# Kernel optimization log

Hardware: AMD Instinct MI355X
Metric: run time of the kernel (lower is better)

Reference implementation:

```python
import jax, jax.numpy as jnp
import numpy as np

PROP_TIME = 8  # matches init kwarg prop_time


def setup_inputs() -> dict:
    key = jax.random.key(0)
    k1, k2, k3, k4, k5 = jax.random.split(key, 5)
    B, H, W = 8, 480, 640
    return {
        "guided1": jax.random.normal(k1, (B, 9, H, W), dtype=jnp.float32),
        "guided2": jax.random.normal(k2, (B, 9, H, W), dtype=jnp.float32),
        "guided3": jax.random.normal(k3, (B, 9, H, W), dtype=jnp.float32),
        "fuse": jax.random.uniform(k4, (B, 3, H, W), dtype=jnp.float32),
        "x": jax.random.normal(k5, (B, 1, H, W), dtype=jnp.float32),
    }


def _neighbors(x, d):
    """Gather the 3x3 dilated neighborhood of a [B,1,H,W] map -> [B,9,H,W].
    Equivalent to F.unfold(x, 3, dilation=d, padding=d) reshaped to spatial."""
    B, _, H, W = x.shape
    xp = jnp.pad(x[:, 0], ((0, 0), (d, d), (d, d)))  # B, H+2d, W+2d
    return jnp.stack(
        [xp[:, i * d:i * d + H, j * d:j * d + W] for i in range(3) for j in range(3)],
        axis=1,
    )


def reference(guided1, guided2, guided3, fuse, x):
    # per-pixel affinity kernels, normalized over the 9 taps
    k1 = jax.nn.softmax(guided1, axis=1)
    k2 = jax.nn.softmax(guided2, axis=1)
    k3 = jax.nn.softmax(guided3, axis=1)
    f1, f2, f3 = fuse[:, 0:1], fuse[:, 1:2], fuse[:, 2:3]
    for _ in range(PROP_TIME):
        o1 = jnp.sum(_neighbors(x, 1) * k1, axis=1, keepdims=True)  # B,1,H,W
        o2 = jnp.sum(_neighbors(x, 2) * k2, axis=1, keepdims=True)
        o3 = jnp.sum(_neighbors(x, 3) * k3, axis=1, keepdims=True)
        x = o1 * f1 + o2 * f2 + o3 * f3
    return x
```

## Files before the change

### kernel.cpp

```cpp
#include <hip/hip_runtime.h>

constexpr int B_ = 8;
constexpr int H_ = 480;
constexpr int W_ = 640;
constexpr int HW = H_ * W_;
constexpr int N  = B_ * HW;

__global__ __launch_bounds__(256) void wprep_kernel(
    const float* __restrict__ g1, const float* __restrict__ g2,
    const float* __restrict__ g3, const float* __restrict__ fuse,
    _Float16* __restrict__ w)
{
    const int j  = blockIdx.x * 64 + (threadIdx.x & 63);
    const int i  = blockIdx.y * 4  + (threadIdx.x >> 6);
    const int z  = blockIdx.z;
    const int b  = z / 3;
    const int d  = z - b * 3;
    const int hw = i * W_ + j;
    const int p  = b * HW + hw;

    const float* gs[3] = {g1, g2, g3};
    const float* gb = gs[d] + (size_t)b * 9 * HW + hw;

    float e[9];
    float m = -1e30f;
#pragma unroll
    for (int c = 0; c < 9; ++c) {
        e[c] = gb[(size_t)c * HW];
        m = fmaxf(m, e[c]);
    }
    float s = 0.f;
#pragma unroll
    for (int c = 0; c < 9; ++c) {
        e[c] = __expf(e[c] - m);
        s += e[c];
    }
    const float f = fuse[((size_t)b * 3 + d) * HW + hw] / s;
#pragma unroll
    for (int c = 0; c < 9; ++c)
        w[(size_t)(d * 9 + c) * N + p] = (_Float16)(e[c] * f);
}

__global__ __launch_bounds__(256) void prop_kernel(
    const float* __restrict__ xin, const _Float16* __restrict__ w,
    float* __restrict__ xout)
{
    const int j  = blockIdx.x * 64 + (threadIdx.x & 63);
    const int i  = blockIdx.y * 4  + (threadIdx.x >> 6);
    const int b  = blockIdx.z;
    const int hw = i * W_ + j;
    const int p  = b * HW + hw;

    const float* xb = xin + (size_t)b * HW;
    float acc = 0.f;
#pragma unroll
    for (int d = 1; d <= 3; ++d) {
#pragma unroll
        for (int ki = 0; ki < 3; ++ki) {
            const int ii = i + (ki - 1) * d;
            const bool vi = (unsigned)ii < (unsigned)H_;
#pragma unroll
            for (int kj = 0; kj < 3; ++kj) {
                const int jj = j + (kj - 1) * d;
                float xv = 0.f;
                if (vi && (unsigned)jj < (unsigned)W_)
                    xv = xb[ii * W_ + jj];
                const int plane = (d - 1) * 9 + ki * 3 + kj;
                acc = fmaf(xv, (float)w[(size_t)plane * N + p], acc);
            }
        }
    }
    xout[p] = acc;
}

extern "C" void kernel_launch(void* const* d_in, const int* in_sizes, int n_in,
                              void* d_out, int out_size, void* d_ws, size_t ws_size,
                              hipStream_t stream)
{
    const float* g1   = (const float*)d_in[0];
    const float* g2   = (const float*)d_in[1];
    const float* g3   = (const float*)d_in[2];
    const float* fuse = (const float*)d_in[3];
    const float* x    = (const float*)d_in[4];
    float* out = (float*)d_out;

    char* ws = (char*)d_ws;
    _Float16* w = (_Float16*)ws;
    float* xa = (float*)(ws + (size_t)27 * N * 2);
    float* xb = xa + N;

    const dim3 block(256);
    wprep_kernel<<<dim3(W_ / 64, H_ / 4, B_ * 3), block, 0, stream>>>(g1, g2, g3, fuse, w);

    const dim3 pgrid(W_ / 64, H_ / 4, B_);
    const float* src = x;
    float* bufs[2] = {xa, xb};
    for (int t = 0; t < 8; ++t) {
        float* dst = (t == 7) ? out : bufs[t & 1];
        prop_kernel<<<pgrid, block, 0, stream>>>(src, w, dst);
        src = dst;
    }
}
```

Measured before the change: 297.7 us.

## Store per-pixel weights interleaved (28 halves) and load them with vector loads

Changes the weight workspace from 27 planar fp16 planes to a pixel-interleaved layout padded to 28 halves, so each pixel's weights sit contiguously. The prep kernel now computes all three softmaxes per pixel and writes them with 16-byte vector stores. The propagation kernel loads the weights with three 16-byte loads and one 8-byte load instead of 27 scattered 2-byte loads. This cuts the number of memory transactions, but each lane's weight loads are now strided by 56 bytes across the wave, which may reduce coalescing efficiency.

Result: no change. 301.8 us (+1.4%).

```diff
diff --git a/kernel.cpp b/kernel.cpp
--- a/kernel.cpp
+++ b/kernel.cpp
@@ -1,44 +1,56 @@
 #include <hip/hip_runtime.h>
+
+typedef __attribute__((ext_vector_type(4))) float    float4v;
+typedef __attribute__((ext_vector_type(8))) _Float16 half8v;
+typedef __attribute__((ext_vector_type(4))) _Float16 half4v;
 
 constexpr int B_ = 8;
 constexpr int H_ = 480;
 constexpr int W_ = 640;
 constexpr int HW = H_ * W_;
 constexpr int N  = B_ * HW;
+constexpr int WPP = 28;
 
 __global__ __launch_bounds__(256) void wprep_kernel(
     const float* __restrict__ g1, const float* __restrict__ g2,
     const float* __restrict__ g3, const float* __restrict__ fuse,
     _Float16* __restrict__ w)
 {
-    const int j  = blockIdx.x * 64 + (threadIdx.x & 63);
-    const int i  = blockIdx.y * 4  + (threadIdx.x >> 6);
-    const int z  = blockIdx.z;
-    const int b  = z / 3;
-    const int d  = z - b * 3;
-    const int hw = i * W_ + j;
-    const int p  = b * HW + hw;
+    const int p  = blockIdx.x * 256 + threadIdx.x;
+    const int b  = p / HW;
+    const int hw = p - b * HW;
+
+    _Float16 wl[WPP];
+    wl[27] = (_Float16)0.f;
 
     const float* gs[3] = {g1, g2, g3};
-    const float* gb = gs[d] + (size_t)b * 9 * HW + hw;
+#pragma unroll
+    for (int d = 0; d < 3; ++d) {
+        const float* gb = gs[d] + (size_t)b * 9 * HW + hw;
+        float e[9];
+        float m = -1e30f;
+#pragma unroll
+        for (int c = 0; c < 9; ++c) {
+            e[c] = gb[(size_t)c * HW];
+            m = fmaxf(m, e[c]);
+        }
+        float s = 0.f;
+#pragma unroll
+        for (int c = 0; c < 9; ++c) {
+            e[c] = __expf(e[c] - m);
+            s += e[c];
+        }
+        const float f = fuse[((size_t)b * 3 + d) * HW + hw] / s;
+#pragma unroll
+        for (int c = 0; c < 9; ++c)
+            wl[d * 9 + c] = (_Float16)(e[c] * f);
+    }
 
-    float e[9];
-    float m = -1e30f;
-#pragma unroll
-    for (int c = 0; c < 9; ++c) {
-        e[c] = gb[(size_t)c * HW];
-        m = fmaxf(m, e[c]);
-    }
-    float s = 0.f;
-#pragma unroll
-    for (int c = 0; c < 9; ++c) {
-        e[c] = __expf(e[c] - m);
-        s += e[c];
-    }
-    const float f = fuse[((size_t)b * 3 + d) * HW + hw] / s;
-#pragma unroll
-    for (int c = 0; c < 9; ++c)
-        w[(size_t)(d * 9 + c) * N + p] = (_Float16)(e[c] * f);
+    _Float16* wp = w + (size_t)p * WPP;
+    *(half8v*)(wp + 0)  = *(half8v*)(wl + 0);
+    *(half8v*)(wp + 8)  = *(half8v*)(wl + 8);
+    *(half8v*)(wp + 16) = *(half8v*)(wl + 16);
+    *(half4v*)(wp + 24) = *(half4v*)(wl + 24);
 }
 
 __global__ __launch_bounds__(256) void prop_kernel(
@@ -50,6 +62,18 @@
     const int b  = blockIdx.z;
     const int hw = i * W_ + j;
     const int p  = b * HW + hw;
+
+    const _Float16* wp = w + (size_t)p * WPP;
+    const half8v w0 = *(const half8v*)(wp + 0);
+    const half8v w1 = *(const half8v*)(wp + 8);
+    const half8v w2 = *(const half8v*)(wp + 16);
+    const half4v w3 = *(const half4v*)(wp + 24);
+
+    _Float16 wl[27];
+#pragma unroll
+    for (int k = 0; k < 8; ++k) { wl[k] = w0[k]; wl[8 + k] = w1[k]; wl[16 + k] = w2[k]; }
+#pragma unroll
+    for (int k = 0; k < 3; ++k) wl[24 + k] = w3[k];
 
     const float* xb = xin + (size_t)b * HW;
     float acc = 0.f;
@@ -65,8 +89,7 @@
                 float xv = 0.f;
                 if (vi && (unsigned)jj < (unsigned)W_)
                     xv = xb[ii * W_ + jj];
-                const int plane = (d - 1) * 9 + ki * 3 + kj;
-                acc = fmaf(xv, (float)w[(size_t)plane * N + p], acc);
+                acc = fmaf(xv, (float)wl[(d - 1) * 9 + ki * 3 + kj], acc);
             }
         }
     }
@@ -86,18 +109,17 @@
 
     char* ws = (char*)d_ws;
     _Float16* w = (_Float16*)ws;
-    float* xa = (float*)(ws + (size_t)27 * N * 2);
+    float* xa = (float*)(ws + (size_t)N * WPP * 2);
     float* xb = xa + N;
 
-    const dim3 block(256);
-    wprep_kernel<<<dim3(W_ / 64, H_ / 4, B_ * 3), block, 0, stream>>>(g1, g2, g3, fuse, w);
+    wprep_kernel<<<N / 256, 256, 0, stream>>>(g1, g2, g3, fuse, w);
 
     const dim3 pgrid(W_ / 64, H_ / 4, B_);
     const float* src = x;
     float* bufs[2] = {xa, xb};
     for (int t = 0; t < 8; ++t) {
         float* dst = (t == 7) ? out : bufs[t & 1];
-        prop_kernel<<<pgrid, block, 0, stream>>>(src, w, dst);
+        prop_kernel<<<pgrid, 256, 0, stream>>>(src, w, dst);
         src = dst;
     }
 }
```
